# Kernel optimization log

Hardware: AMD Instinct MI355X
Metric: run time of the kernel (lower is better)

Reference implementation:

```python
import jax, jax.numpy as jnp
import numpy as np

B, S, D = 2048, 200, 64
H1, H2 = 64, 16
EPS = 1e-9
NEG_INF = -2.0**32 + 1.0


def dice(x, alpha, mean, var):
    # Dice activation at inference: BN (no center/scale) with moving stats, then
    # p = sigmoid(x_norm); out = alpha*(1-p)*x + p*x
    xn = (x - mean) * jax.lax.rsqrt(var + EPS)
    p = jax.nn.sigmoid(xn)
    return alpha * (1.0 - p) * x + p * x


def setup_inputs() -> dict:
    key = jax.random.key(0)
    ks = jax.random.split(key, 12)
    query_emb = jax.random.normal(ks[0], (B, D), dtype=jnp.float32)
    key_emb = jax.random.normal(ks[1], (B, S, D), dtype=jnp.float32)
    seq_length = jax.random.randint(ks[2], (B, 1), 1, S + 1, dtype=jnp.int32)
    # attention MLP weights (no bias): 4*D -> H1 -> H2 -> 1
    W1 = jax.random.normal(ks[3], (4 * D, H1), dtype=jnp.float32) * 0.05
    W2 = jax.random.normal(ks[4], (H1, H2), dtype=jnp.float32) * 0.05
    W3 = jax.random.normal(ks[5], (H2, 1), dtype=jnp.float32) * 0.05
    # Dice params: alpha (trainable) + BN moving stats
    alpha1 = jax.random.normal(ks[6], (H1,), dtype=jnp.float32) * 0.1
    mean1 = jax.random.normal(ks[7], (H1,), dtype=jnp.float32) * 0.1
    var1 = jax.random.uniform(ks[8], (H1,), dtype=jnp.float32, minval=0.5, maxval=1.5)
    alpha2 = jax.random.normal(ks[9], (H2,), dtype=jnp.float32) * 0.1
    mean2 = jax.random.normal(ks[10], (H2,), dtype=jnp.float32) * 0.1
    var2 = jax.random.uniform(ks[11], (H2,), dtype=jnp.float32, minval=0.5, maxval=1.5)
    return {
        "query_emb": query_emb, "key_emb": key_emb, "seq_length": seq_length,
        "W1": W1, "alpha1": alpha1, "mean1": mean1, "var1": var1,
        "W2": W2, "alpha2": alpha2, "mean2": mean2, "var2": var2,
        "W3": W3,
    }


def reference(query_emb, key_emb, seq_length, W1, alpha1, mean1, var1,
              W2, alpha2, mean2, var2, W3):
    b, s, d = key_emb.shape
    q = jnp.broadcast_to(query_emb[:, None, :], (b, s, d))
    # (B, S, 4D) interaction features
    att = jnp.concatenate([q, key_emb, q - key_emb, q * key_emb], axis=-1)
    h = dice(att @ W1, alpha1, mean1, var1)           # (B, S, H1)
    h = dice(h @ W2, alpha2, mean2, var2)             # (B, S, H2)
    score = h @ W3                                    # (B, S, 1)
    mask = (jnp.arange(s)[None, :] < seq_length).astype(score.dtype)[..., None]
    score = score * mask + (1.0 - mask) * NEG_INF
    score = jax.nn.sigmoid(score)                     # weight_normalization=False
    return jnp.sum(score * key_emb, axis=1)           # (B, D)
```

## Files before the change

kernel.cpp:

```cpp
#include <hip/hip_runtime.h>

#define NB   2048
#define SEQ  200
#define DIM  64
#define NH1  64
#define NH2  16
#define EPSF 1e-9f
#define ROWS1 4

typedef float fvec4 __attribute__((ext_vector_type(4)));
typedef short svec8 __attribute__((ext_vector_type(8)));

__device__ __forceinline__ short f2bf(float f) {
    unsigned u = __float_as_uint(f);
    u += 0x7fffu + ((u >> 16) & 1u);
    return (short)(u >> 16);
}

__global__ __launch_bounds__(256, 2)
void din_prep_kernel(const float* __restrict__ q,
                     const float* __restrict__ W1,
                     char*  __restrict__ wsA,
                     float* __restrict__ qtermws)
{
    __shared__ float Wsub[4096];
    __shared__ float Wd[4096];
    __shared__ float Wac[4096];
    const int t = threadIdx.x;

    #pragma unroll
    for (int it = 0; it < 16; ++it) {
        const int e = it * 256 + t;
        const int d = e >> 6, h = e & 63;
        const float w1a = W1[d * 64 + h];
        const float w1b = W1[(64 + d) * 64 + h];
        const float w1c = W1[(128 + d) * 64 + h];
        const float w1dv= W1[(192 + d) * 64 + h];
        Wsub[e] = w1b - w1c;
        Wac[e]  = w1a + w1c;
        Wd[e]   = w1dv;
    }
    __syncthreads();

    const int lane = t & 63;
    const int wave = t >> 6;
    const int qd4  = lane >> 4;
    const int m    = lane & 15;

    for (int r = 0; r < ROWS1; ++r) {
        const int b = blockIdx.x * ROWS1 + r;
        const float* qrow = q + (size_t)b * DIM;

        {
            const int h = wave * 16 + m;
            float s = 0.f;
            #pragma unroll
            for (int i = 0; i < 16; ++i) {
                const int d = qd4 * 16 + i;
                s = fmaf(qrow[d], Wac[d * 64 + h], s);
            }
            s += __shfl_xor(s, 16);
            s += __shfl_xor(s, 32);
            if (qd4 == 0) qtermws[(size_t)b * 64 + h] = s;
        }

        #pragma unroll
        for (int kk = 0; kk < 2; ++kk) {
            svec8 f;
            #pragma unroll
            for (int j = 0; j < 8; ++j) {
                const int d = kk * 32 + qd4 * 8 + j;
                const int h = wave * 16 + m;
                f[j] = f2bf(Wsub[d * 64 + h] + qrow[d] * Wd[d * 64 + h]);
            }
            *(svec8*)(wsA + (size_t)b * 8192 + (((wave << 1) + kk) << 10) + lane * 16) = f;
        }
    }
}

__global__ __launch_bounds__(64, 2)
void din_main_kernel(const float* __restrict__ key,
                     const int*   __restrict__ seqlen,
                     const float* __restrict__ W2,
                     const float* __restrict__ alpha1v,
                     const float* __restrict__ mean1v,
                     const float* __restrict__ var1v,
                     const float* __restrict__ alpha2v,
                     const float* __restrict__ mean2v,
                     const float* __restrict__ var2v,
                     const float* __restrict__ W3,
                     const char*  __restrict__ wsA,
                     const float* __restrict__ qtermws,
                     float* __restrict__ out)
{
    __shared__ short h1w[16 * NH1];
    __shared__ float wsw[16];

    const int b    = blockIdx.x;
    const int lane = threadIdx.x;
    const int qd4  = lane >> 4;
    const int m    = lane & 15;

    int nseq = seqlen[b];
    nseq = nseq < SEQ ? nseq : SEQ;

    svec8 wcf[4][2];
    {
        const char* fb = wsA + (size_t)b * 8192 + (size_t)lane * 16;
        #pragma unroll
        for (int c = 0; c < 4; ++c)
            #pragma unroll
            for (int kk = 0; kk < 2; ++kk)
                wcf[c][kk] = *(const svec8*)(fb + (((c << 1) + kk) << 10));
    }
    float qtermv[4];
    #pragma unroll
    for (int c = 0; c < 4; ++c) qtermv[c] = qtermws[(size_t)b * 64 + c * 16 + m];

    svec8 w2f[2];
    #pragma unroll
    for (int kk = 0; kk < 2; ++kk) {
        svec8 f;
        #pragma unroll
        for (int j = 0; j < 8; ++j)
            f[j] = f2bf(W2[(kk * 32 + qd4 * 8 + j) * NH2 + m]);
        w2f[kk] = f;
    }

    float a1v[4], m1v[4], r1v[4];
    #pragma unroll
    for (int c = 0; c < 4; ++c) {
        a1v[c] = alpha1v[c * 16 + m];
        m1v[c] = mean1v[c * 16 + m];
        r1v[c] = rsqrtf(var1v[c * 16 + m] + EPSF);
    }
    const float a2s = alpha2v[m];
    const float m2s = mean2v[m];
    const float r2s = rsqrtf(var2v[m] + EPSF);
    const float w3s = W3[m];

    fvec4 oacc0 = {0.f,0.f,0.f,0.f}, oacc1 = {0.f,0.f,0.f,0.f};
    fvec4 oacc2 = {0.f,0.f,0.f,0.f}, oacc3 = {0.f,0.f,0.f,0.f};

    const int ntiles = (nseq + 15) >> 4;
    const float* kbase = key + (size_t)b * SEQ * DIM + qd4 * 8;

    fvec4 nv0, nv1, nv2, nv3;
    {
        const float* kp = kbase + (size_t)m * DIM;
        nv0 = *(const fvec4*)(kp);
        nv1 = *(const fvec4*)(kp + 4);
        nv2 = *(const fvec4*)(kp + 32);
        nv3 = *(const fvec4*)(kp + 36);
    }

    for (int tile = 0; tile < ntiles; ++tile) {
        const fvec4 kv0 = nv0, kv1 = nv1, kv2 = nv2, kv3 = nv3;
        if (tile + 1 < ntiles) {
            int row = (tile + 1) * 16 + m;
            row = row < SEQ ? row : SEQ - 1;
            const float* kp = kbase + (size_t)row * DIM;
            nv0 = *(const fvec4*)(kp);
            nv1 = *(const fvec4*)(kp + 4);
            nv2 = *(const fvec4*)(kp + 32);
            nv3 = *(const fvec4*)(kp + 36);
        }

        svec8 af0, af1;
        #pragma unroll
        for (int j = 0; j < 4; ++j) {
            af0[j]     = f2bf(kv0[j]);
            af0[4 + j] = f2bf(kv1[j]);
            af1[j]     = f2bf(kv2[j]);
            af1[4 + j] = f2bf(kv3[j]);
        }

        #pragma unroll
        for (int c = 0; c < 4; ++c) {
            fvec4 acc = (fvec4){0.f, 0.f, 0.f, 0.f};
            acc = __builtin_amdgcn_mfma_f32_16x16x32_bf16(af0, wcf[c][0], acc, 0, 0, 0);
            acc = __builtin_amdgcn_mfma_f32_16x16x32_bf16(af1, wcf[c][1], acc, 0, 0, 0);
            #pragma unroll
            for (int reg = 0; reg < 4; ++reg) {
                const float x  = acc[reg] + qtermv[c];
                const float xn = (x - m1v[c]) * r1v[c];
                const float p  = 1.f / (1.f + __expf(-xn));
                const float h1 = x * (a1v[c] + p * (1.f - a1v[c]));
                h1w[(qd4 * 4 + reg) * NH1 + c * 16 + m] = f2bf(h1);
            }
        }

        const svec8 b0 = *(const svec8*)(h1w + m * NH1 + qd4 * 8);
        const svec8 b1 = *(const svec8*)(h1w + m * NH1 + 32 + qd4 * 8);
        fvec4 acc2 = (fvec4){0.f, 0.f, 0.f, 0.f};
        acc2 = __builtin_amdgcn_mfma_f32_16x16x32_bf16(b0, w2f[0], acc2, 0, 0, 0);
        acc2 = __builtin_amdgcn_mfma_f32_16x16x32_bf16(b1, w2f[1], acc2, 0, 0, 0);

        #pragma unroll
        for (int reg = 0; reg < 4; ++reg) {
            const float x  = acc2[reg];
            const float xn = (x - m2s) * r2s;
            const float p  = 1.f / (1.f + __expf(-xn));
            const float hd = x * (a2s + p * (1.f - a2s));
            float s = hd * w3s;
            s += __shfl_xor(s, 1);
            s += __shfl_xor(s, 2);
            s += __shfl_xor(s, 4);
            s += __shfl_xor(s, 8);
            if (m == 0) {
                const int rg = tile * 16 + qd4 * 4 + reg;
                wsw[qd4 * 4 + reg] = (rg < nseq) ? 1.f / (1.f + __expf(-s)) : 0.f;
            }
        }

        const float w = wsw[m];
        oacc0 += w * kv0;
        oacc1 += w * kv1;
        oacc2 += w * kv2;
        oacc3 += w * kv3;
    }

    #pragma unroll
    for (int e = 0; e < 4; ++e) {
        float v0 = oacc0[e], v1 = oacc1[e], v2 = oacc2[e], v3 = oacc3[e];
        #pragma unroll
        for (int msk = 1; msk < 16; msk <<= 1) {
            v0 += __shfl_xor(v0, msk);
            v1 += __shfl_xor(v1, msk);
            v2 += __shfl_xor(v2, msk);
            v3 += __shfl_xor(v3, msk);
        }
        oacc0[e] = v0; oacc1[e] = v1; oacc2[e] = v2; oacc3[e] = v3;
    }
    if (m == 0) {
        float* op = out + (size_t)b * DIM + qd4 * 8;
        *(fvec4*)(op)      = oacc0;
        *(fvec4*)(op + 4)  = oacc1;
        *(fvec4*)(op + 32) = oacc2;
        *(fvec4*)(op + 36) = oacc3;
    }
}

extern "C" void kernel_launch(void* const* d_in, const int* in_sizes, int n_in,
                              void* d_out, int out_size, void* d_ws, size_t ws_size,
                              hipStream_t stream) {
    const float* q      = (const float*)d_in[0];
    const float* key    = (const float*)d_in[1];
    const int*   seqlen = (const int*)d_in[2];
    const float* W1     = (const float*)d_in[3];
    const float* alpha1 = (const float*)d_in[4];
    const float* mean1  = (const float*)d_in[5];
    const float* var1   = (const float*)d_in[6];
    const float* W2     = (const float*)d_in[7];
    const float* alpha2 = (const float*)d_in[8];
    const float* mean2  = (const float*)d_in[9];
    const float* var2   = (const float*)d_in[10];
    const float* W3     = (const float*)d_in[11];
    float* out          = (float*)d_out;

    char*  wsA     = (char*)d_ws;
    float* qtermws = (float*)((char*)d_ws + (size_t)NB * 8192);

    din_prep_kernel<<<NB / ROWS1, 256, 0, stream>>>(q, W1, wsA, qtermws);
    din_main_kernel<<<NB, 64, 0, stream>>>(key, seqlen, W2,
                                           alpha1, mean1, var1,
                                           alpha2, mean2, var2,
                                           W3, wsA, qtermws, out);
}
```

Baseline: 192.3 us.

## Split sequence tiles across two waves per batch row and drop LDS score buffer

The main kernel now launches two waves per batch row, and each wave handles alternating 16-row tiles with its own LDS scratch. Partial outputs are merged through shared memory after a barrier. The explicit software prefetch of the next key tile is removed. The query term is folded into the MFMA accumulator's initial value. Per-row scores are now spread across lanes with shuffles instead of an LDS round trip. The aim is more parallelism and shorter per-row latency. The cost is duplicated per-wave setup loads (weight fragments, qterm) and an extra block-level sync and reduction.

```diff
diff --git a/kernel.cpp b/kernel.cpp
--- a/kernel.cpp
+++ b/kernel.cpp
@@ -78,7 +78,7 @@
     }
 }
 
-__global__ __launch_bounds__(64, 2)
+__global__ __launch_bounds__(128, 4)
 void din_main_kernel(const float* __restrict__ key,
                      const int*   __restrict__ seqlen,
                      const float* __restrict__ W2,
@@ -93,13 +93,17 @@
                      const float* __restrict__ qtermws,
                      float* __restrict__ out)
 {
-    __shared__ short h1w[16 * NH1];
-    __shared__ float wsw[16];
+    __shared__ short h1base[2][16 * NH1];
+    __shared__ float obuf[2 * 64];
 
     const int b    = blockIdx.x;
-    const int lane = threadIdx.x;
+    const int t    = threadIdx.x;
+    const int lane = t & 63;
+    const int wave = __builtin_amdgcn_readfirstlane(t >> 6);
     const int qd4  = lane >> 4;
     const int m    = lane & 15;
+
+    short* h1w = h1base[wave];
 
     int nseq = seqlen[b];
     nseq = nseq < SEQ ? nseq : SEQ;
@@ -145,26 +149,14 @@
     const int ntiles = (nseq + 15) >> 4;
     const float* kbase = key + (size_t)b * SEQ * DIM + qd4 * 8;
 
-    fvec4 nv0, nv1, nv2, nv3;
-    {
-        const float* kp = kbase + (size_t)m * DIM;
-        nv0 = *(const fvec4*)(kp);
-        nv1 = *(const fvec4*)(kp + 4);
-        nv2 = *(const fvec4*)(kp + 32);
-        nv3 = *(const fvec4*)(kp + 36);
-    }
-
-    for (int tile = 0; tile < ntiles; ++tile) {
-        const fvec4 kv0 = nv0, kv1 = nv1, kv2 = nv2, kv3 = nv3;
-        if (tile + 1 < ntiles) {
-            int row = (tile + 1) * 16 + m;
-            row = row < SEQ ? row : SEQ - 1;
-            const float* kp = kbase + (size_t)row * DIM;
-            nv0 = *(const fvec4*)(kp);
-            nv1 = *(const fvec4*)(kp + 4);
-            nv2 = *(const fvec4*)(kp + 32);
-            nv3 = *(const fvec4*)(kp + 36);
-        }
+    for (int tile = wave; tile < ntiles; tile += 2) {
+        int row = tile * 16 + m;
+        row = row < SEQ ? row : SEQ - 1;
+        const float* kp = kbase + (size_t)row * DIM;
+        const fvec4 kv0 = *(const fvec4*)(kp);
+        const fvec4 kv1 = *(const fvec4*)(kp + 4);
+        const fvec4 kv2 = *(const fvec4*)(kp + 32);
+        const fvec4 kv3 = *(const fvec4*)(kp + 36);
 
         svec8 af0, af1;
         #pragma unroll
@@ -177,12 +169,13 @@
 
         #pragma unroll
         for (int c = 0; c < 4; ++c) {
-            fvec4 acc = (fvec4){0.f, 0.f, 0.f, 0.f};
+            const float qt = qtermv[c];
+            fvec4 acc = (fvec4){qt, qt, qt, qt};
             acc = __builtin_amdgcn_mfma_f32_16x16x32_bf16(af0, wcf[c][0], acc, 0, 0, 0);
             acc = __builtin_amdgcn_mfma_f32_16x16x32_bf16(af1, wcf[c][1], acc, 0, 0, 0);
             #pragma unroll
             for (int reg = 0; reg < 4; ++reg) {
-                const float x  = acc[reg] + qtermv[c];
+                const float x  = acc[reg];
                 const float xn = (x - m1v[c]) * r1v[c];
                 const float p  = 1.f / (1.f + __expf(-xn));
                 const float h1 = x * (a1v[c] + p * (1.f - a1v[c]));
@@ -196,24 +189,35 @@
         acc2 = __builtin_amdgcn_mfma_f32_16x16x32_bf16(b0, w2f[0], acc2, 0, 0, 0);
         acc2 = __builtin_amdgcn_mfma_f32_16x16x32_bf16(b1, w2f[1], acc2, 0, 0, 0);
 
+        float sreg[4];
         #pragma unroll
         for (int reg = 0; reg < 4; ++reg) {
             const float x  = acc2[reg];
             const float xn = (x - m2s) * r2s;
             const float p  = 1.f / (1.f + __expf(-xn));
             const float hd = x * (a2s + p * (1.f - a2s));
-            float s = hd * w3s;
-            s += __shfl_xor(s, 1);
-            s += __shfl_xor(s, 2);
-            s += __shfl_xor(s, 4);
-            s += __shfl_xor(s, 8);
-            if (m == 0) {
-                const int rg = tile * 16 + qd4 * 4 + reg;
-                wsw[qd4 * 4 + reg] = (rg < nseq) ? 1.f / (1.f + __expf(-s)) : 0.f;
-            }
-        }
-
-        const float w = wsw[m];
+            sreg[reg] = hd * w3s;
+        }
+        #pragma unroll
+        for (int msk = 1; msk < 16; msk <<= 1) {
+            sreg[0] += __shfl_xor(sreg[0], msk);
+            sreg[1] += __shfl_xor(sreg[1], msk);
+            sreg[2] += __shfl_xor(sreg[2], msk);
+            sreg[3] += __shfl_xor(sreg[3], msk);
+        }
+        const int src = (m >> 2) << 4;
+        const float s0b = __shfl(sreg[0], src);
+        const float s1b = __shfl(sreg[1], src);
+        const float s2b = __shfl(sreg[2], src);
+        const float s3b = __shfl(sreg[3], src);
+        const float sa = (m & 1) ? s1b : s0b;
+        const float sb = (m & 1) ? s3b : s2b;
+        const float sv = (m & 2) ? sb : sa;
+
+        const int   rg = tile * 16 + m;
+        const float pw = 1.f / (1.f + __expf(-sv));
+        const float w  = (rg < nseq) ? pw : 0.f;
+
         oacc0 += w * kv0;
         oacc1 += w * kv1;
         oacc2 += w * kv2;
@@ -233,12 +237,15 @@
         oacc0[e] = v0; oacc1[e] = v1; oacc2[e] = v2; oacc3[e] = v3;
     }
     if (m == 0) {
-        float* op = out + (size_t)b * DIM + qd4 * 8;
+        float* op = obuf + wave * 64 + qd4 * 8;
         *(fvec4*)(op)      = oacc0;
         *(fvec4*)(op + 4)  = oacc1;
         *(fvec4*)(op + 32) = oacc2;
         *(fvec4*)(op + 36) = oacc3;
     }
+    __syncthreads();
+    if (t < 64)
+        out[(size_t)b * DIM + t] = obuf[t] + obuf[64 + t];
 }
 
 extern "C" void kernel_launch(void* const* d_in, const int* in_sizes, int n_in,
@@ -262,8 +269,8 @@
     float* qtermws = (float*)((char*)d_ws + (size_t)NB * 8192);
 
     din_prep_kernel<<<NB / ROWS1, 256, 0, stream>>>(q, W1, wsA, qtermws);
-    din_main_kernel<<<NB, 64, 0, stream>>>(key, seqlen, W2,
-                                           alpha1, mean1, var1,
-                                           alpha2, mean2, var2,
-                                           W3, wsA, qtermws, out);
-}
+    din_main_kernel<<<NB, 128, 0, stream>>>(key, seqlen, W2,
+                                            alpha1, mean1, var1,
+                                            alpha2, mean2, var2,
+                                            W3, wsA, qtermws, out);
+}
```

Measured after the change: 198.1 us. 1.03x slower.
